# Kernel tuning notes

Hardware: AMD Instinct MI355X
Metric: run time of the kernel (lower is better)

Reference implementation:

```python
import jax, jax.numpy as jnp
import numpy as np

T, B, A, OBS = 128, 16, 32, 256
K, NACT, HID = 3, 9, 32


def setup_inputs() -> dict:
    key = jax.random.key(0)
    ks = jax.random.split(key, 12)
    sc = 0.1  # small init scale for stability
    d = {}
    d["x"] = jax.random.normal(ks[0], (T, B, A, OBS), jnp.float32)
    d["done"] = jax.random.randint(ks[1], (T, B), 0, 2, jnp.int32)
    d["actions"] = jax.random.randint(ks[2], (T, B, A, K), 0, NACT, jnp.int32)
    d["W1"] = sc * jax.random.normal(ks[3], (128, OBS), jnp.float32)
    d["b1"] = jnp.zeros((128,), jnp.float32)
    d["W2"] = sc * jax.random.normal(ks[4], (128, 128), jnp.float32)
    d["b2"] = jnp.zeros((128,), jnp.float32)
    d["W3"] = sc * jax.random.normal(ks[5], (64, 128), jnp.float32)
    d["b3"] = jnp.zeros((64,), jnp.float32)
    d["Wih"] = sc * jax.random.normal(ks[6], (4 * HID, 64), jnp.float32)
    d["Whh"] = sc * jax.random.normal(ks[7], (4 * HID, HID), jnp.float32)
    d["bih"] = jnp.zeros((4 * HID,), jnp.float32)
    d["bhh"] = jnp.zeros((4 * HID,), jnp.float32)
    d["Wh"] = sc * jax.random.normal(ks[8], (K, NACT, HID), jnp.float32)
    d["bh"] = jnp.zeros((K, NACT), jnp.float32)
    d["h0"] = jnp.zeros((B * A, HID), jnp.float32)
    d["c0"] = jnp.zeros((B * A, HID), jnp.float32)
    return d


def _forward(x, done, actions, W1, b1, W2, b2, W3, b3,
             Wih, Whh, bih, bhh, Wh, bh, h0, c0):
    # MLP trunk: n_obs -> 128 -> 128 -> 64 (tanh, tanh, linear)
    z = jnp.tanh(x @ W1.T + b1)
    z = jnp.tanh(z @ W2.T + b2)
    z = z @ W3.T + b3                       # [T, B, A, 64]
    zf = z.reshape(T, B * A, 64)
    # done[t] repeated per agent (repeat_interleave along batch*agent axis)
    done_f = jnp.repeat(done.astype(x.dtype), A, axis=1)  # [T, B*A]

    def step(carry, inp):
        h, c = carry
        zt, dt = inp                        # [B*A,64], [B*A]
        mask = (1.0 - dt)[:, None]
        h = h * mask
        c = c * mask
        gates = zt @ Wih.T + bih + h @ Whh.T + bhh  # [B*A, 4H]
        i, f, g, o = jnp.split(gates, 4, axis=-1)   # PyTorch gate order i,f,g,o
        i, f, o = jax.nn.sigmoid(i), jax.nn.sigmoid(f), jax.nn.sigmoid(o)
        g = jnp.tanh(g)
        c = f * c + i * g
        h = o * jnp.tanh(c)
        return (h, c), h

    (_, _), ys = jax.lax.scan(step, (h0, c0), (zf, done_f))
    y = ys.reshape(T, B, A, HID)
    # multi-head categorical logits: stacked heads [K, NACT, HID]
    logits = jnp.einsum('tbah,knh->tbakn', y, Wh) + bh  # [T,B,A,K,NACT]
    lp = jax.nn.log_softmax(logits, axis=-1)
    entropies = -jnp.sum(jnp.exp(lp) * lp, axis=-1)     # [T,B,A,K]
    alp = jnp.take_along_axis(lp, actions[..., None], axis=-1)[..., 0]  # [T,B,A,K]
    logprobs = jnp.prod(alp, axis=-1)  # faithful: product of per-head log-probs
    return logprobs, entropies


def reference(x, done, actions, W1, b1, W2, b2, W3, b3,
              Wih, Whh, bih, bhh, Wh, bh, h0, c0):
    logprobs, entropies = _forward(x, done, actions, W1, b1, W2, b2, W3, b3,
                                   Wih, Whh, bih, bhh, Wh, bh, h0, c0)
    return actions, logprobs, entropies
```

## Files before the change

kernel.cpp:

```cpp
#include <hip/hip_runtime.h>
#include <math.h>

namespace {
constexpr int Tn = 128, Bn = 16, An = 32, OBS = 256, Kh = 3, NACT = 9, HID = 32;
constexpr int TBA = Tn * Bn * An;
constexpr int BA  = Bn * An;
constexpr int OUT_LP  = TBA * Kh;
constexpr int OUT_ENT = TBA * Kh + TBA;

constexpr int W1_OFF  = 0;
constexpr int W2_OFF  = 32768;
constexpr int W3_OFF  = 49152;
constexpr int WIH_OFF = 57344;
constexpr int W16_TOT = 65536;

typedef __fp16   pk16x2 __attribute__((ext_vector_type(2)));
typedef _Float16 half8v __attribute__((ext_vector_type(8)));
typedef float    f32x4  __attribute__((ext_vector_type(4)));
}

__device__ __forceinline__ float fast_sig(float x) {
  return __builtin_amdgcn_rcpf(1.f + __expf(-x));
}
__device__ __forceinline__ float fast_tanh(float x) {
  return fmaf(2.f, fast_sig(2.f * x), -1.f);
}
__device__ __forceinline__ unsigned h2bits(pk16x2 h) {
  return __builtin_bit_cast(unsigned, h);
}
__device__ __forceinline__ pk16x2 bits2h(unsigned u) {
  return __builtin_bit_cast(pk16x2, u);
}
__device__ __forceinline__ float dot2(pk16x2 a, pk16x2 b, float c) {
#if __has_builtin(__builtin_amdgcn_fdot2)
  return __builtin_amdgcn_fdot2(a, b, c, false);
#else
  c = fmaf((float)a.x, (float)b.x, c);
  return fmaf((float)a.y, (float)b.y, c);
#endif
}
__device__ __forceinline__ float dpp_swap1(float x) {
  return __uint_as_float((unsigned)__builtin_amdgcn_mov_dpp(
      (int)__float_as_uint(x), 0xB1, 0xF, 0xF, true));
}

__global__ __launch_bounds__(256) void cvtw_act_kernel(
    const float* __restrict__ W1, const float* __restrict__ W2,
    const float* __restrict__ W3, const float* __restrict__ Wih,
    _Float16* __restrict__ w16, const int* __restrict__ actions,
    float* __restrict__ out)
{
  const int bid = blockIdx.x;
  if (bid < W16_TOT/256) {
    int i = bid * 256 + threadIdx.x;
    float v;
    if (i < W2_OFF)       v = W1[i];
    else if (i < W3_OFF)  v = W2[i - W2_OFF];
    else if (i < WIH_OFF) v = W3[i - W3_OFF];
    else                  v = Wih[i - WIH_OFF];
    w16[i] = (_Float16)v;
  } else {
    int i = (bid - W16_TOT/256) * 256 + threadIdx.x;
    out[i] = (float)actions[i];
  }
}

template<int ROWS, int WSTR>
__device__ __forceinline__ void stage_wh(const _Float16* __restrict__ Wg, int kofs,
                                         _Float16* __restrict__ wt, int tid)
{
#pragma unroll
  for (int it = 0; it < ROWS/64; ++it) {
    int idx = tid + it*512;
    int o = idx >> 3, g8 = idx & 7;
    *(half8v*)&wt[o*72 + g8*8] =
        *(const half8v*)&Wg[(size_t)o*WSTR + kofs + g8*8];
  }
}

template<int NOC, int XSTR>
__device__ __forceinline__ void mfma_slab(const _Float16* __restrict__ xsrc,
                                          const _Float16* __restrict__ wt,
                                          int rA, int ln, int quad, f32x4 acc[8])
{
#pragma unroll
  for (int kc = 0; kc < 2; ++kc) {
    half8v a = *(const half8v*)&xsrc[rA*XSTR + kc*32 + quad*8];
#pragma unroll
    for (int oc = 0; oc < NOC; ++oc) {
      half8v b = *(const half8v*)&wt[(oc*16 + ln)*72 + kc*32 + quad*8];
      acc[oc] = __builtin_amdgcn_mfma_f32_16x16x32_f16(a, b, acc[oc], 0, 0, 0);
    }
  }
}

__global__ __launch_bounds__(512) void mlp_kernel(
    const float* __restrict__ x, const _Float16* __restrict__ w16,
    const float* __restrict__ b1, const float* __restrict__ b2,
    const float* __restrict__ b3, const float* __restrict__ bih,
    const float* __restrict__ bhh, uint2* __restrict__ G1q)
{
  __shared__ __align__(16) _Float16 xs[128*72];
  __shared__ __align__(16) _Float16 wt[128*72];
  __shared__ __align__(16) _Float16 act[128*136];
  const _Float16* W1h  = w16 + W1_OFF;
  const _Float16* W2h  = w16 + W2_OFF;
  const _Float16* W3h  = w16 + W3_OFF;
  const _Float16* Wihh = w16 + WIH_OFF;
  const int tid  = threadIdx.x;
  const int w    = tid >> 6;
  const int lane = tid & 63;
  const int ln   = lane & 15;
  const int quad = lane >> 4;
  const int rA   = 16*w + ln;
  const int r0   = 16*w + quad*4;
  const int R0   = blockIdx.x * 128;
  f32x4 acc[8];

#pragma unroll
  for (int oc = 0; oc < 8; ++oc) acc[oc] = (f32x4)0.f;
  for (int kt = 0; kt < 4; ++kt) {
#pragma unroll
    for (int it = 0; it < 2; ++it) {
      int idx = tid + it*512;
      int r = idx >> 3, g8 = idx & 7;
      const float* xp = &x[(size_t)(R0 + r)*OBS + kt*64 + g8*8];
      float4 v0 = *(const float4*)xp;
      float4 v1 = *(const float4*)(xp + 4);
      half8v hv = { (_Float16)v0.x, (_Float16)v0.y, (_Float16)v0.z, (_Float16)v0.w,
                    (_Float16)v1.x, (_Float16)v1.y, (_Float16)v1.z, (_Float16)v1.w };
      *(half8v*)&xs[r*72 + g8*8] = hv;
    }
    stage_wh<128, 256>(W1h, kt*64, wt, tid);
    __syncthreads();
    mfma_slab<8, 72>(xs, wt, rA, ln, quad, acc);
    __syncthreads();
  }
#pragma unroll
  for (int oc = 0; oc < 8; ++oc) {
    int o = oc*16 + ln;
    float bv = b1[o];
#pragma unroll
    for (int r = 0; r < 4; ++r)
      act[(r0 + r)*136 + o] = (_Float16)fast_tanh(acc[oc][r] + bv);
  }

#pragma unroll
  for (int oc = 0; oc < 8; ++oc) acc[oc] = (f32x4)0.f;
  for (int kt = 0; kt < 2; ++kt) {
    stage_wh<128, 128>(W2h, kt*64, wt, tid);
    __syncthreads();
    mfma_slab<8, 136>(act + kt*64, wt, rA, ln, quad, acc);
    __syncthreads();
  }
#pragma unroll
  for (int oc = 0; oc < 8; ++oc) {
    int o = oc*16 + ln;
    float bv = b2[o];
#pragma unroll
    for (int r = 0; r < 4; ++r)
      act[(r0 + r)*136 + o] = (_Float16)fast_tanh(acc[oc][r] + bv);
  }

#pragma unroll
  for (int oc = 0; oc < 4; ++oc) acc[oc] = (f32x4)0.f;
  for (int kt = 0; kt < 2; ++kt) {
    stage_wh<64, 128>(W3h, kt*64, wt, tid);
    __syncthreads();
    mfma_slab<4, 136>(act + kt*64, wt, rA, ln, quad, acc);
    __syncthreads();
  }
#pragma unroll
  for (int oc = 0; oc < 4; ++oc) {
    int o = oc*16 + ln;
    float bv = b3[o];
#pragma unroll
    for (int r = 0; r < 4; ++r)
      xs[(r0 + r)*72 + o] = (_Float16)(acc[oc][r] + bv);
  }

#pragma unroll
  for (int oc = 0; oc < 8; ++oc) acc[oc] = (f32x4)0.f;
  stage_wh<128, 64>(Wihh, 0, wt, tid);
  __syncthreads();
  mfma_slab<8, 72>(xs, wt, rA, ln, quad, acc);
#pragma unroll
  for (int p = 0; p < 2; ++p) {
    int ui = p*16 + ln;
    float bi = bih[ui]      + bhh[ui];
    float bf = bih[ui + 32] + bhh[ui + 32];
    float bg = bih[ui + 64] + bhh[ui + 64];
    float bo = bih[ui + 96] + bhh[ui + 96];
#pragma unroll
    for (int r = 0; r < 4; ++r) {
      int n = R0 + r0 + r;
      uint2 q;
      q.x = h2bits(__builtin_amdgcn_cvt_pkrtz(acc[p  ][r] + bi, acc[p+4][r] + bg));
      q.y = h2bits(__builtin_amdgcn_cvt_pkrtz(acc[p+2][r] + bf, acc[p+6][r] + bo));
      G1q[(size_t)n*32 + ui] = q;
    }
  }
}

__global__ __launch_bounds__(64) void lstm_kernel(
    const uint2* __restrict__ G1q, const float* __restrict__ Whh,
    const int* __restrict__ done, const float* __restrict__ h0,
    const float* __restrict__ c0, unsigned* __restrict__ Y16)
{
  const int lane = threadIdx.x;
  const int u    = lane & 31;
  const int half = lane >> 5;
  const int row  = blockIdx.x;
  const int b    = row >> 5;

  pk16x2 wA[16], wB[16];
  const int rwA = u + half*32;
#pragma unroll
  for (int k4 = 0; k4 < 8; ++k4) {
    float4 a  = *(const float4*)&Whh[(rwA     )*HID + k4*4];
    float4 bq = *(const float4*)&Whh[(rwA + 64)*HID + k4*4];
    wA[2*k4+0] = __builtin_amdgcn_cvt_pkrtz(a.x,  a.y);
    wA[2*k4+1] = __builtin_amdgcn_cvt_pkrtz(a.z,  a.w);
    wB[2*k4+0] = __builtin_amdgcn_cvt_pkrtz(bq.x, bq.y);
    wB[2*k4+1] = __builtin_amdgcn_cvt_pkrtz(bq.z, bq.w);
  }

  unsigned long long dm0 = __ballot(done[lane*Bn + b] != 0);
  unsigned long long dm1 = __ballot(done[(lane + 64)*Bn + b] != 0);

  float c = c0[row*HID + u];
  float h = h0[row*HID + u];
  unsigned pk = h2bits(__builtin_amdgcn_cvt_pkrtz(h, dpp_swap1(h)));

  const float sSc = half ? 1.f : 2.f;
  const float m1c = half ? 1.f : 2.f;
  const float m0c = half ? 0.f : -1.f;

  const unsigned* gb = (const unsigned*)G1q + ((size_t)row*32 + u)*2 + half;
  const size_t gstride = (size_t)BA * 64;
  unsigned q0  = gb[ 0*gstride];
  unsigned q1  = gb[ 1*gstride];
  unsigned q2  = gb[ 2*gstride];
  unsigned q3  = gb[ 3*gstride];
  unsigned q4  = gb[ 4*gstride];
  unsigned q5  = gb[ 5*gstride];
  unsigned q6  = gb[ 6*gstride];
  unsigned q7  = gb[ 7*gstride];
  unsigned q8  = gb[ 8*gstride];
  unsigned q9  = gb[ 9*gstride];
  unsigned q10 = gb[10*gstride];
  unsigned q11 = gb[11*gstride];
  unsigned q12 = gb[12*gstride];
  unsigned q13 = gb[13*gstride];
  unsigned q14 = gb[14*gstride];
  unsigned q15 = gb[15*gstride];

#define LSTM_PHASE(TT, Q)                                                \
  {                                                                      \
    unsigned cur = Q;                                                    \
    int tnx = (TT) + 16; tnx = (tnx < Tn) ? tnx : (Tn - 1);              \
    Q = gb[(size_t)tnx * gstride];                                       \
    unsigned long long dbit = ((TT) < 64) ? (dm0 >> (TT))                \
                                          : (dm1 >> ((TT) - 64));        \
    float m = (dbit & 1ull) ? 0.f : 1.f;         \
    unsigned hp[16];                                                     \
    _Pragma("unroll") for (int k = 0; k < 16; ++k)                       \
      hp[k] = __builtin_amdgcn_readlane(pk, 2*k);                        \
    float aA0=0.f, aA1=0.f, aB0=0.f, aB1=0.f;                            \
    _Pragma("unroll") for (int k = 0; k < 16; k += 2) {                  \
      pk16x2 ha = bits2h(hp[k]), hb = bits2h(hp[k+1]);                   \
      aA0 = dot2(wA[k], ha, aA0); aA1 = dot2(wA[k+1], hb, aA1);          \
      aB0 = dot2(wB[k], ha, aB0); aB1 = dot2(wB[k+1], hb, aB1);          \
    }                                                                    \
    pk16x2 g2 = bits2h(cur);                                             \
    float x0 = fmaf(m, aA0 + aA1, (float)g2.x);               \
    float x1 = fmaf(m, aB0 + aB1, (float)g2.y);               \
    float v0 = fast_sig(x0);                                             \
    float v1 = fmaf(m1c, fast_sig(sSc * x1), m0c);                       \
    float o0 = __shfl_xor(v0, 32, 64);                                   \
    float o1 = __shfl_xor(v1, 32, 64);                                   \
    float iv = half ? o0 : v0;                                           \
    float fv = half ? v0 : o0;                                           \
    float gv = half ? o1 : v1;                                           \
    float ov = half ? v1 : o1;                                           \
    c = fmaf(fv, m * c, iv * gv);                                        \
    h = ov * fast_tanh(c);                                               \
    pk = h2bits(__builtin_amdgcn_cvt_pkrtz(h, dpp_swap1(h)));            \
    if ((lane & 33) == 0)                                                \
      Y16[((size_t)(TT)*BA + row)*16 + (u >> 1)] = pk;                   \
  }

  for (int t = 0; t < Tn; t += 16) {
    LSTM_PHASE(t +  0, q0)
    LSTM_PHASE(t +  1, q1)
    LSTM_PHASE(t +  2, q2)
    LSTM_PHASE(t +  3, q3)
    LSTM_PHASE(t +  4, q4)
    LSTM_PHASE(t +  5, q5)
    LSTM_PHASE(t +  6, q6)
    LSTM_PHASE(t +  7, q7)
    LSTM_PHASE(t +  8, q8)
    LSTM_PHASE(t +  9, q9)
    LSTM_PHASE(t + 10, q10)
    LSTM_PHASE(t + 11, q11)
    LSTM_PHASE(t + 12, q12)
    LSTM_PHASE(t + 13, q13)
    LSTM_PHASE(t + 14, q14)
    LSTM_PHASE(t + 15, q15)
  }
#undef LSTM_PHASE
}

__global__ __launch_bounds__(256) void head_kernel(
    const unsigned* __restrict__ Y16, const float* __restrict__ Wh,
    const float* __restrict__ bh, const int* __restrict__ actions,
    float* __restrict__ out)
{
  __shared__ __align__(16) float whs[27*32];
  __shared__ float bhs[32];
  const int tid = threadIdx.x;
  const int R0 = blockIdx.x * 256;
  for (int i = tid; i < 27*32; i += 256) whs[i] = Wh[i];
  if (tid < 27) bhs[tid] = bh[tid];
  const int row = R0 + tid;
  float yv[32];
#pragma unroll
  for (int i4 = 0; i4 < 4; ++i4) {
    uint4 yw = *(const uint4*)&Y16[(size_t)row*16 + i4*4];
    pk16x2 p0 = bits2h(yw.x), p1 = bits2h(yw.y), p2 = bits2h(yw.z), p3 = bits2h(yw.w);
    yv[i4*8+0] = (float)p0.x; yv[i4*8+1] = (float)p0.y;
    yv[i4*8+2] = (float)p1.x; yv[i4*8+3] = (float)p1.y;
    yv[i4*8+4] = (float)p2.x; yv[i4*8+5] = (float)p2.y;
    yv[i4*8+6] = (float)p3.x; yv[i4*8+7] = (float)p3.y;
  }
  __syncthreads();
  float l[27];
#pragma unroll
  for (int m = 0; m < 27; ++m) {
    float a = bhs[m];
#pragma unroll
    for (int k4 = 0; k4 < 8; ++k4) {
      float4 w4 = *(const float4*)&whs[m*32 + k4*4];
      a = fmaf(yv[k4*4+0], w4.x, a);
      a = fmaf(yv[k4*4+1], w4.y, a);
      a = fmaf(yv[k4*4+2], w4.z, a);
      a = fmaf(yv[k4*4+3], w4.w, a);
    }
    l[m] = a;
  }
  float logprob = 1.0f;
#pragma unroll
  for (int kk = 0; kk < 3; ++kk) {
    float mx = l[kk*9];
#pragma unroll
    for (int n = 1; n < 9; ++n) mx = fmaxf(mx, l[kk*9+n]);
    float s = 0.f;
#pragma unroll
    for (int n = 0; n < 9; ++n) s += __expf(l[kk*9+n] - mx);
    float lse = mx + __logf(s);
    float ent = 0.f;
#pragma unroll
    for (int n = 0; n < 9; ++n) {
      float lp = l[kk*9+n] - lse;
      ent -= __expf(lp) * lp;
    }
    int a = actions[row*3 + kk];
    float alp = 0.f;
#pragma unroll
    for (int n = 0; n < 9; ++n) alp = (a == n) ? (l[kk*9+n] - lse) : alp;
    logprob *= alp;
    out[OUT_ENT + row*3 + kk] = ent;
  }
  out[OUT_LP + row] = logprob;
}

extern "C" void kernel_launch(void* const* d_in, const int* in_sizes, int n_in,
                              void* d_out, int out_size, void* d_ws, size_t ws_size,
                              hipStream_t stream)
{
  const float* x       = (const float*)d_in[0];
  const int*   done    = (const int*)  d_in[1];
  const int*   actions = (const int*)  d_in[2];
  const float* W1  = (const float*)d_in[3];
  const float* b1  = (const float*)d_in[4];
  const float* W2  = (const float*)d_in[5];
  const float* b2  = (const float*)d_in[6];
  const float* W3  = (const float*)d_in[7];
  const float* b3  = (const float*)d_in[8];
  const float* Wih = (const float*)d_in[9];
  const float* Whh = (const float*)d_in[10];
  const float* bih = (const float*)d_in[11];
  const float* bhh = (const float*)d_in[12];
  const float* Wh  = (const float*)d_in[13];
  const float* bh  = (const float*)d_in[14];
  const float* h0  = (const float*)d_in[15];
  const float* c0  = (const float*)d_in[16];
  float* out = (float*)d_out;

  uint2* G1q = (uint2*)d_ws;
  unsigned* Y16 = (unsigned*)(G1q + (size_t)TBA*32);
  _Float16* W16 = (_Float16*)(Y16 + (size_t)TBA*16);

  cvtw_act_kernel<<<W16_TOT/256 + (TBA*Kh)/256, 256, 0, stream>>>(
      W1, W2, W3, Wih, W16, actions, out);
  mlp_kernel<<<TBA/128, 512, 0, stream>>>(x, W16, b1, b2, b3, bih, bhh, G1q);
  lstm_kernel<<<BA, 64, 0, stream>>>(G1q, Whh, done, h0, c0, Y16);
  head_kernel<<<TBA/256, 256, 0, stream>>>(Y16, Wh, bh, actions, out);
}
```

Measured before the change: 187.1 us.

## Split LSTM recurrence into time chunks that restart at episode resets

```diff
diff --git a/kernel.cpp b/kernel.cpp
--- a/kernel.cpp
+++ b/kernel.cpp
@@ -7,6 +7,8 @@
 constexpr int BA  = Bn * An;
 constexpr int OUT_LP  = TBA * Kh;
 constexpr int OUT_ENT = TBA * Kh + TBA;
+constexpr int NCHUNK = 8;
+constexpr int CHUNKW = Tn / NCHUNK;
 
 constexpr int W1_OFF  = 0;
 constexpr int W2_OFF  = 32768;
@@ -42,6 +44,14 @@
 __device__ __forceinline__ float dpp_swap1(float x) {
   return __uint_as_float((unsigned)__builtin_amdgcn_mov_dpp(
       (int)__float_as_uint(x), 0xB1, 0xF, 0xF, true));
+}
+__device__ __forceinline__ int first_done_ge(unsigned long long dm0,
+                                             unsigned long long dm1, int n) {
+  unsigned long long m0 = (n < 64) ? (dm0 & (~0ull << n)) : 0ull;
+  unsigned long long m1 = (n < 64) ? dm1 : (dm1 & (~0ull << (n - 64)));
+  if (m0) return __builtin_ctzll(m0);
+  if (m1) return 64 + __builtin_ctzll(m1);
+  return 128;
 }
 
 __global__ __launch_bounds__(256) void cvtw_act_kernel(
@@ -207,11 +217,21 @@
     const int* __restrict__ done, const float* __restrict__ h0,
     const float* __restrict__ c0, unsigned* __restrict__ Y16)
 {
+  static_assert(BA == 512 && NCHUNK == 8, "index math below assumes 512x8");
   const int lane = threadIdx.x;
   const int u    = lane & 31;
   const int half = lane >> 5;
-  const int row  = blockIdx.x;
+  const int row  = blockIdx.x & (BA - 1);
+  const int ck   = blockIdx.x >> 9;
   const int b    = row >> 5;
+
+  unsigned long long dm0 = __ballot(done[lane*Bn + b] != 0);
+  unsigned long long dm1 = __ballot(done[(lane + 64)*Bn + b] != 0);
+
+  const int s = (ck == 0) ? 0 : first_done_ge(dm0, dm1, ck * CHUNKW);
+  const int e = (ck == NCHUNK - 1) ? Tn
+                                   : first_done_ge(dm0, dm1, (ck + 1) * CHUNKW);
+  if (s >= e) return;
 
   pk16x2 wA[16], wB[16];
   const int rwA = u + half*32;
@@ -225,11 +245,9 @@
     wB[2*k4+1] = __builtin_amdgcn_cvt_pkrtz(bq.z, bq.w);
   }
 
-  unsigned long long dm0 = __ballot(done[lane*Bn + b] != 0);
-  unsigned long long dm1 = __ballot(done[(lane + 64)*Bn + b] != 0);
-
-  float c = c0[row*HID + u];
-  float h = h0[row*HID + u];
+  float c, h;
+  if (ck == 0) { c = c0[row*HID + u]; h = h0[row*HID + u]; }
+  else         { c = 0.f;             h = 0.f; }
   unsigned pk = h2bits(__builtin_amdgcn_cvt_pkrtz(h, dpp_swap1(h)));
 
   const float sSc = half ? 1.f : 2.f;
@@ -238,77 +256,44 @@
 
   const unsigned* gb = (const unsigned*)G1q + ((size_t)row*32 + u)*2 + half;
   const size_t gstride = (size_t)BA * 64;
-  unsigned q0  = gb[ 0*gstride];
-  unsigned q1  = gb[ 1*gstride];
-  unsigned q2  = gb[ 2*gstride];
-  unsigned q3  = gb[ 3*gstride];
-  unsigned q4  = gb[ 4*gstride];
-  unsigned q5  = gb[ 5*gstride];
-  unsigned q6  = gb[ 6*gstride];
-  unsigned q7  = gb[ 7*gstride];
-  unsigned q8  = gb[ 8*gstride];
-  unsigned q9  = gb[ 9*gstride];
-  unsigned q10 = gb[10*gstride];
-  unsigned q11 = gb[11*gstride];
-  unsigned q12 = gb[12*gstride];
-  unsigned q13 = gb[13*gstride];
-  unsigned q14 = gb[14*gstride];
-  unsigned q15 = gb[15*gstride];
-
-#define LSTM_PHASE(TT, Q)                                                \
-  {                                                                      \
-    unsigned cur = Q;                                                    \
-    int tnx = (TT) + 16; tnx = (tnx < Tn) ? tnx : (Tn - 1);              \
-    Q = gb[(size_t)tnx * gstride];                                       \
-    unsigned long long dbit = ((TT) < 64) ? (dm0 >> (TT))                \
-                                          : (dm1 >> ((TT) - 64));        \
-    float m = (dbit & 1ull) ? 0.f : 1.f;         \
-    unsigned hp[16];                                                     \
-    _Pragma("unroll") for (int k = 0; k < 16; ++k)                       \
-      hp[k] = __builtin_amdgcn_readlane(pk, 2*k);                        \
-    float aA0=0.f, aA1=0.f, aB0=0.f, aB1=0.f;                            \
-    _Pragma("unroll") for (int k = 0; k < 16; k += 2) {                  \
-      pk16x2 ha = bits2h(hp[k]), hb = bits2h(hp[k+1]);                   \
-      aA0 = dot2(wA[k], ha, aA0); aA1 = dot2(wA[k+1], hb, aA1);          \
-      aB0 = dot2(wB[k], ha, aB0); aB1 = dot2(wB[k+1], hb, aB1);          \
-    }                                                                    \
-    pk16x2 g2 = bits2h(cur);                                             \
-    float x0 = fmaf(m, aA0 + aA1, (float)g2.x);               \
-    float x1 = fmaf(m, aB0 + aB1, (float)g2.y);               \
-    float v0 = fast_sig(x0);                                             \
-    float v1 = fmaf(m1c, fast_sig(sSc * x1), m0c);                       \
-    float o0 = __shfl_xor(v0, 32, 64);                                   \
-    float o1 = __shfl_xor(v1, 32, 64);                                   \
-    float iv = half ? o0 : v0;                                           \
-    float fv = half ? v0 : o0;                                           \
-    float gv = half ? o1 : v1;                                           \
-    float ov = half ? v1 : o1;                                           \
-    c = fmaf(fv, m * c, iv * gv);                                        \
-    h = ov * fast_tanh(c);                                               \
-    pk = h2bits(__builtin_amdgcn_cvt_pkrtz(h, dpp_swap1(h)));            \
-    if ((lane & 33) == 0)                                                \
-      Y16[((size_t)(TT)*BA + row)*16 + (u >> 1)] = pk;                   \
-  }
-
-  for (int t = 0; t < Tn; t += 16) {
-    LSTM_PHASE(t +  0, q0)
-    LSTM_PHASE(t +  1, q1)
-    LSTM_PHASE(t +  2, q2)
-    LSTM_PHASE(t +  3, q3)
-    LSTM_PHASE(t +  4, q4)
-    LSTM_PHASE(t +  5, q5)
-    LSTM_PHASE(t +  6, q6)
-    LSTM_PHASE(t +  7, q7)
-    LSTM_PHASE(t +  8, q8)
-    LSTM_PHASE(t +  9, q9)
-    LSTM_PHASE(t + 10, q10)
-    LSTM_PHASE(t + 11, q11)
-    LSTM_PHASE(t + 12, q12)
-    LSTM_PHASE(t + 13, q13)
-    LSTM_PHASE(t + 14, q14)
-    LSTM_PHASE(t + 15, q15)
-  }
-#undef LSTM_PHASE
+
+  unsigned qcur = gb[(size_t)s * gstride];
+  for (int t = s; t < e; ++t) {
+    int tn = t + 1; tn = (tn < e) ? tn : (e - 1);
+    unsigned qnext = gb[(size_t)tn * gstride];
+
+    unsigned long long dbit = (t < 64) ? (dm0 >> t) : (dm1 >> (t - 64));
+    float m = (dbit & 1ull) ? 0.f : 1.f;
+    unsigned hp[16];
+#pragma unroll
+    for (int k = 0; k < 16; ++k)
+      hp[k] = __builtin_amdgcn_readlane(pk, 2*k);
+    float aA0 = 0.f, aA1 = 0.f, aB0 = 0.f, aB1 = 0.f;
+#pragma unroll
+    for (int k = 0; k < 16; k += 2) {
+      pk16x2 ha = bits2h(hp[k]), hb = bits2h(hp[k+1]);
+      aA0 = dot2(wA[k], ha, aA0); aA1 = dot2(wA[k+1], hb, aA1);
+      aB0 = dot2(wB[k], ha, aB0); aB1 = dot2(wB[k+1], hb, aB1);
+    }
+    pk16x2 g2 = bits2h(qcur);
+    float x0 = fmaf(m, aA0 + aA1, (float)g2.x);
+    float x1 = fmaf(m, aB0 + aB1, (float)g2.y);
+    float v0 = fast_sig(x0);
+    float v1 = fmaf(m1c, fast_sig(sSc * x1), m0c);
+    float o0 = __shfl_xor(v0, 32, 64);
+    float o1 = __shfl_xor(v1, 32, 64);
+    float iv = half ? o0 : v0;
+    float fv = half ? v0 : o0;
+    float gv = half ? o1 : v1;
+    float ov = half ? v1 : o1;
+    c = fmaf(fv, m * c, iv * gv);
+    h = ov * fast_tanh(c);
+    pk = h2bits(__builtin_amdgcn_cvt_pkrtz(h, dpp_swap1(h)));
+    if ((lane & 33) == 0)
+      Y16[((size_t)t*BA + row)*16 + (u >> 1)] = pk;
+
+    qcur = qnext;
+  }
 }
 
 __global__ __launch_bounds__(256) void head_kernel(
@@ -404,6 +389,6 @@
   cvtw_act_kernel<<<W16_TOT/256 + (TBA*Kh)/256, 256, 0, stream>>>(
       W1, W2, W3, Wih, W16, actions, out);
   mlp_kernel<<<TBA/128, 512, 0, stream>>>(x, W16, b1, b2, b3, bih, bhh, G1q);
-  lstm_kernel<<<BA, 64, 0, stream>>>(G1q, Whh, done, h0, c0, Y16);
+  lstm_kernel<<<BA * NCHUNK, 64, 0, stream>>>(G1q, Whh, done, h0, c0, Y16);
   head_kernel<<<TBA/256, 256, 0, stream>>>(Y16, Wh, bh, actions, out);
 }
```

Result: faster. 172.4 us (-7.8%).
